# Performance work log

Measured on AMD Instinct MI355X. Metric: run time of the kernel, lower is better.

Reference implementation:

```python
import jax, jax.numpy as jnp
import numpy as np

B, S, W = 64, 128, 20
VOCAB, E, H = 256, 64, 256


def setup_inputs() -> dict:
    key = jax.random.key(0)
    ks = jax.random.split(key, 10)
    return {
        "chars": jax.random.randint(ks[0], (B, S, W), 0, VOCAB),
        "emb": jax.random.uniform(ks[1], (VOCAB, E), jnp.float32, -0.32, 0.32),
        "w1": jax.random.normal(ks[2], (H, E, 1), jnp.float32) * 0.1,
        "b1": jax.random.normal(ks[3], (H,), jnp.float32) * 0.1,
        "w3": jax.random.normal(ks[4], (H, E, 3), jnp.float32) * 0.1,
        "b3": jax.random.normal(ks[5], (H,), jnp.float32) * 0.1,
        "w5": jax.random.normal(ks[6], (H, E, 5), jnp.float32) * 0.1,
        "b5": jax.random.normal(ks[7], (H,), jnp.float32) * 0.1,
        "lw": jax.random.normal(ks[8], (H, 3 * H), jnp.float32) * 0.05,
        "lb": jax.random.normal(ks[9], (H,), jnp.float32) * 0.05,
    }


def _conv_relu_maxpool(x, w, b):
    # x: [N, E, W], w: [H, E, k] ('same' padding k//2) -> [N, H]
    k = w.shape[-1]
    pad = k // 2
    y = jax.lax.conv_general_dilated(
        x, w, window_strides=(1,), padding=[(pad, pad)],
        dimension_numbers=("NCH", "OIH", "NCH"))
    y = jax.nn.relu(y + b[None, :, None])
    return jnp.max(y, axis=2)  # global max over char positions


def reference(chars, emb, w1, b1, w3, b3, w5, b5, lw, lb):
    b, s, wlen = chars.shape
    flat = chars.reshape(-1, wlen)                 # [N, W]
    x = emb[flat]                                  # [N, W, E]
    x = jnp.transpose(x, (0, 2, 1))                # [N, E, W]
    outs = jnp.concatenate([
        _conv_relu_maxpool(x, w1, b1),
        _conv_relu_maxpool(x, w3, b3),
        _conv_relu_maxpool(x, w5, b5),
    ], axis=1)                                     # [N, 3H]
    out = outs @ lw.T + lb                         # [N, H]
    return out.reshape(b, s, -1)
```

## Files before the change

### kernel.cpp

```cpp
#include <hip/hip_runtime.h>
#include <hip/hip_bf16.h>

#define BB 64
#define SS 128
#define WW 20
#define NW (BB*SS)
#define VOCAB 256
#define EE 64
#define HH 256
#define K3 (3*HH)
#define NTAP 9
#define UNIT 2304

typedef short bf16x8 __attribute__((ext_vector_type(8)));
typedef float f32x4  __attribute__((ext_vector_type(4)));

__device__ __forceinline__ ushort f2bs(float x) {
    __hip_bfloat16 h = __float2bfloat16(x);
    union { __hip_bfloat16 h; ushort u; } c; c.h = h; return c.u;
}
__device__ __forceinline__ float blo(unsigned u) {
    union { unsigned i; float f; } c; c.i = u << 16; return c.f;
}
__device__ __forceinline__ float bhi(unsigned u) {
    union { unsigned i; float f; } c; c.i = u & 0xffff0000u; return c.f;
}

#define SET4(d, w0, w1) { d[0]=blo(w0); d[1]=bhi(w0); d[2]=blo(w1); d[3]=bhi(w1); }
#define ADD4(d, w0, w1) { d[0]+=blo(w0); d[1]+=bhi(w0); d[2]+=blo(w1); d[3]+=bhi(w1); }
#define MAX4(m, s) { m[0]=fmaxf(m[0],s[0]); m[1]=fmaxf(m[1],s[1]); \
                     m[2]=fmaxf(m[2],s[2]); m[3]=fmaxf(m[3],s[3]); }


__global__ __launch_bounds__(256) void prep(
        const float* __restrict__ w1,
        const float* __restrict__ w3,
        const float* __restrict__ w5,
        const float* __restrict__ lw,
        float* __restrict__ wTp,
        ushort* __restrict__ lwb) {
    const int bid = blockIdx.x;
    if (bid < 576) {
        int idx = bid * 256 + threadIdx.x;
        int e = idx / UNIT;
        int j = idx - e * UNIT;
        int tap, h;
        if (j < 2048) {
            int chunk = j >> 9, w = j & 511, p = w & 7;
            tap = chunk * 2 + (p >> 2);
            h   = (w >> 3) * 4 + (p & 3);
        } else { tap = 8; h = j - 2048; }
        float v;
        if (tap == 0)      v = w1[h*EE + e];
        else if (tap <= 3) v = w3[(h*EE + e)*3 + (tap-1)];
        else               v = w5[(h*EE + e)*5 + (tap-4)];
        wTp[idx] = v;
    } else {
        int i = ((bid - 576) * 256 + threadIdx.x) * 4;
        float4 v = *(const float4*)(lw + i);
        ushort4 o;
        o.x = f2bs(v.x); o.y = f2bs(v.y); o.z = f2bs(v.z); o.w = f2bs(v.w);
        *(ushort4*)(lwb + i) = o;
    }
}

__global__ __launch_bounds__(256) void build_tables(
        const float* __restrict__ emb,
        const float* __restrict__ wTp,
        ushort* __restrict__ P2) {
    __shared__ float emb_s[2][EE];
    const int v0 = blockIdx.x * 2;
    const int j  = blockIdx.y * 256 + threadIdx.x;
    const int t  = threadIdx.x;
    if (t < 2*EE) emb_s[t >> 6][t & 63] = emb[v0*EE + t];
    __syncthreads();

    float a0 = 0.f, a1 = 0.f;
    const float* wp = wTp + j;
    #pragma unroll 8
    for (int e = 0; e < EE; ++e) {
        float w = wp[e * UNIT];
        a0 += emb_s[0][e] * w;
        a1 += emb_s[1][e] * w;
    }
    P2[(size_t)(v0+0)*UNIT + j] = f2bs(a0);
    P2[(size_t)(v0+1)*UNIT + j] = f2bs(a1);
}

__global__ __launch_bounds__(256) void conv_pool(
        const int* __restrict__ chars,
        const ushort* __restrict__ P2,
        const float* __restrict__ b1,
        const float* __restrict__ b3,
        const float* __restrict__ b5,
        ushort* __restrict__ outs) {
    const int tid  = threadIdx.x;
    const int wave = tid >> 6, lane = tid & 63;
    const int n    = blockIdx.x * 4 + wave;
    const char* Pb = (const char*)P2;

    const int* cp = chars + n * WW;
    int c[WW];
    #pragma unroll
    for (int j = 0; j < WW; ++j) c[j] = __builtin_amdgcn_readfirstlane(cp[j]);

    float acc3[3][4], acc5[5][4], m1[4], m3[4], m5[4];
    #pragma unroll
    for (int i = 0; i < 4; ++i) {
        acc3[0][i] = 0.f; acc5[0][i] = 0.f; acc5[1][i] = 0.f;
        m1[i] = -1e30f; m3[i] = -1e30f; m5[i] = -1e30f;
    }

    uint4 q[2][4]; uint2 e8[2];
    {
        const char* p = Pb + (size_t)c[0] * 4608;
        #pragma unroll
        for (int i = 0; i < 4; ++i) q[0][i] = *(const uint4*)(p + i*1024 + lane*16);
        e8[0] = *(const uint2*)(p + 4096 + lane*8);
    }

    #pragma unroll
    for (int j = 0; j < WW; ++j) {
        const int cur = j & 1, nxt = cur ^ 1;
        if (j + 1 < WW) {
            const char* p = Pb + (size_t)c[j+1] * 4608;
            #pragma unroll
            for (int i = 0; i < 4; ++i) q[nxt][i] = *(const uint4*)(p + i*1024 + lane*16);
            e8[nxt] = *(const uint2*)(p + 4096 + lane*8);
        }
        uint4 q0 = q[cur][0], q1 = q[cur][1], q2 = q[cur][2], q3 = q[cur][3];
        uint2 ee = e8[cur];

        m1[0] = fmaxf(m1[0], blo(q0.x)); m1[1] = fmaxf(m1[1], bhi(q0.x));
        m1[2] = fmaxf(m1[2], blo(q0.y)); m1[3] = fmaxf(m1[3], bhi(q0.y));
        if (j + 1 < WW) SET4(acc3[(j+1)%3], q0.z, q0.w)
        ADD4(acc3[j%3], q1.x, q1.y)
        if (j >= 1) { ADD4(acc3[(j-1)%3], q1.z, q1.w)
                      MAX4(m3, acc3[(j-1)%3]) }
        if (j + 2 < WW) SET4(acc5[(j+2)%5], q2.x, q2.y)
        if (j + 1 < WW) ADD4(acc5[(j+1)%5], q2.z, q2.w)
        ADD4(acc5[j%5], q3.x, q3.y)
        if (j >= 1) ADD4(acc5[(j-1)%5], q3.z, q3.w)
        if (j >= 2) { ADD4(acc5[(j-2)%5], ee.x, ee.y)
                      MAX4(m5, acc5[(j-2)%5]) }
    }
    MAX4(m3, acc3[(WW-1)%3])
    MAX4(m5, acc5[(WW-2)%5])
    MAX4(m5, acc5[(WW-1)%5])

    const int h4 = lane * 4;
    float4 bb1 = *(const float4*)(b1 + h4);
    float4 bb3 = *(const float4*)(b3 + h4);
    float4 bb5 = *(const float4*)(b5 + h4);
    ushort* op = outs + (size_t)n * K3 + h4;
    ushort4 o;
    o.x = f2bs(fmaxf(m1[0]+bb1.x, 0.f)); o.y = f2bs(fmaxf(m1[1]+bb1.y, 0.f));
    o.z = f2bs(fmaxf(m1[2]+bb1.z, 0.f)); o.w = f2bs(fmaxf(m1[3]+bb1.w, 0.f));
    *(ushort4*)(op + 0*HH) = o;
    o.x = f2bs(fmaxf(m3[0]+bb3.x, 0.f)); o.y = f2bs(fmaxf(m3[1]+bb3.y, 0.f));
    o.z = f2bs(fmaxf(m3[2]+bb3.z, 0.f)); o.w = f2bs(fmaxf(m3[3]+bb3.w, 0.f));
    *(ushort4*)(op + 1*HH) = o;
    o.x = f2bs(fmaxf(m5[0]+bb5.x, 0.f)); o.y = f2bs(fmaxf(m5[1]+bb5.y, 0.f));
    o.z = f2bs(fmaxf(m5[2]+bb5.z, 0.f)); o.w = f2bs(fmaxf(m5[3]+bb5.w, 0.f));
    *(ushort4*)(op + 2*HH) = o;
}

__global__ __launch_bounds__(64) void gemm_out(
        const ushort* __restrict__ outs,
        const ushort* __restrict__ lwb,
        const float* __restrict__ lb,
        float* __restrict__ out) {
    const int lane = threadIdx.x;
    const int m0 = blockIdx.x * 32;
    const int n0 = blockIdx.y * 32;
    const int mrow = lane & 15, quad = lane >> 4;

    f32x4 acc00 = (f32x4){0,0,0,0}, acc01 = (f32x4){0,0,0,0};
    f32x4 acc10 = (f32x4){0,0,0,0}, acc11 = (f32x4){0,0,0,0};
    const ushort* ap = outs + (size_t)(m0 + mrow) * K3 + quad * 8;
    const ushort* bp = lwb  + (size_t)(n0 + mrow) * K3 + quad * 8;

    bf16x8 a0 = *(const bf16x8*)ap, a1 = *(const bf16x8*)(ap + 16*K3);
    bf16x8 b0 = *(const bf16x8*)bp, b1 = *(const bf16x8*)(bp + 16*K3);

    #pragma unroll
    for (int it = 0; it < K3/32; ++it) {
        const int kn = (it + 1 < K3/32) ? (it + 1) * 32 : 0;
        bf16x8 a0n = *(const bf16x8*)(ap + kn);
        bf16x8 a1n = *(const bf16x8*)(ap + 16*K3 + kn);
        bf16x8 b0n = *(const bf16x8*)(bp + kn);
        bf16x8 b1n = *(const bf16x8*)(bp + 16*K3 + kn);
        acc00 = __builtin_amdgcn_mfma_f32_16x16x32_bf16(a0, b0, acc00, 0, 0, 0);
        acc01 = __builtin_amdgcn_mfma_f32_16x16x32_bf16(a0, b1, acc01, 0, 0, 0);
        acc10 = __builtin_amdgcn_mfma_f32_16x16x32_bf16(a1, b0, acc10, 0, 0, 0);
        acc11 = __builtin_amdgcn_mfma_f32_16x16x32_bf16(a1, b1, acc11, 0, 0, 0);
        a0 = a0n; a1 = a1n; b0 = b0n; b1 = b1n;
    }

    #pragma unroll
    for (int i = 0; i < 2; ++i) {
        #pragma unroll
        for (int jn = 0; jn < 2; ++jn) {
            const f32x4 acc = (i==0) ? (jn==0 ? acc00 : acc01)
                                     : (jn==0 ? acc10 : acc11);
            int ncol = n0 + jn*16 + mrow;
            float lbv = lb[ncol];
            #pragma unroll
            for (int r = 0; r < 4; ++r)
                out[(size_t)(m0 + i*16 + quad*4 + r)*HH + ncol] = acc[r] + lbv;
        }
    }
}

extern "C" void kernel_launch(void* const* d_in, const int* in_sizes, int n_in,
                              void* d_out, int out_size, void* d_ws, size_t ws_size,
                              hipStream_t stream) {
    const int*   chars = (const int*)d_in[0];
    const float* emb   = (const float*)d_in[1];
    const float* w1    = (const float*)d_in[2];
    const float* b1    = (const float*)d_in[3];
    const float* w3    = (const float*)d_in[4];
    const float* b3    = (const float*)d_in[5];
    const float* w5    = (const float*)d_in[6];
    const float* b5    = (const float*)d_in[7];
    const float* lw    = (const float*)d_in[8];
    const float* lb    = (const float*)d_in[9];

    ushort* P2   = (ushort*)d_ws;
    float*  wTp  = (float*)(P2 + VOCAB * UNIT);
    ushort* outs = (ushort*)(wTp + EE * UNIT);
    ushort* lwb  = outs + (size_t)NW * K3;

    prep<<<768, 256, 0, stream>>>(w1, w3, w5, lw, wTp, lwb);
    build_tables<<<dim3(VOCAB/2, NTAP), 256, 0, stream>>>(emb, wTp, P2);
    conv_pool<<<NW/4, 256, 0, stream>>>(chars, P2, b1, b3, b5, outs);
    gemm_out<<<dim3(NW/32, HH/32), 64, 0, stream>>>(outs, lwb, lb, (float*)d_out);
}
```

Measured before the change: 141.5 us.

## Split conv_pool channels across two waves per word and shrink GEMM tiles

Reorders the precomputed per-character tap table into two 128-channel halves so each word is handled by two waves, each producing two channels per lane instead of four. Character indices are loaded with one vector load plus readlane, and the kernel gets an occupancy hint. build_tables now processes four vocab rows per block. The output GEMM uses 16-row tiles to launch more blocks. The aim is more parallelism and lower register pressure, at the cost of more waves reading the same character data and less reuse of B per GEMM block.

```diff
diff --git a/kernel.cpp b/kernel.cpp
--- a/kernel.cpp
+++ b/kernel.cpp
@@ -1,14 +1,12 @@
 #include <hip/hip_runtime.h>
 #include <hip/hip_bf16.h>
 
-#define BB 64
-#define SS 128
 #define WW 20
-#define NW (BB*SS)
+#define NW 8192
 #define VOCAB 256
 #define EE 64
 #define HH 256
-#define K3 (3*HH)
+#define K3 768
 #define NTAP 9
 #define UNIT 2304
 
@@ -25,11 +23,13 @@
 __device__ __forceinline__ float bhi(unsigned u) {
     union { unsigned i; float f; } c; c.i = u & 0xffff0000u; return c.f;
 }
-
-#define SET4(d, w0, w1) { d[0]=blo(w0); d[1]=bhi(w0); d[2]=blo(w1); d[3]=bhi(w1); }
-#define ADD4(d, w0, w1) { d[0]+=blo(w0); d[1]+=bhi(w0); d[2]+=blo(w1); d[3]+=bhi(w1); }
-#define MAX4(m, s) { m[0]=fmaxf(m[0],s[0]); m[1]=fmaxf(m[1],s[1]); \
-                     m[2]=fmaxf(m[2],s[2]); m[3]=fmaxf(m[3],s[3]); }
+__device__ __forceinline__ unsigned pack2(float lo, float hi) {
+    return (unsigned)f2bs(lo) | ((unsigned)f2bs(hi) << 16);
+}
+
+#define SET2(d, w) { d[0] = blo(w); d[1] = bhi(w); }
+#define ADD2(d, w) { d[0] += blo(w); d[1] += bhi(w); }
+#define MAX2(m, s) { m[0] = fmaxf(m[0], s[0]); m[1] = fmaxf(m[1], s[1]); }
 
 
 __global__ __launch_bounds__(256) void prep(
@@ -44,12 +44,14 @@
         int idx = bid * 256 + threadIdx.x;
         int e = idx / UNIT;
         int j = idx - e * UNIT;
+        int o  = j / 1152;
+        int jh = j - o * 1152;
         int tap, h;
-        if (j < 2048) {
-            int chunk = j >> 9, w = j & 511, p = w & 7;
-            tap = chunk * 2 + (p >> 2);
-            h   = (w >> 3) * 4 + (p & 3);
-        } else { tap = 8; h = j - 2048; }
+        if (jh < 1024) {
+            int c = jh >> 8, q = jh & 255, u = q >> 2, p = q & 3;
+            tap = 2*c + (p >> 1);
+            h   = o*128 + 2*u + (p & 1);
+        } else { tap = 8; h = o*128 + (jh - 1024); }
         float v;
         if (tap == 0)      v = w1[h*EE + e];
         else if (tap <= 3) v = w3[(h*EE + e)*3 + (tap-1)];
@@ -58,111 +60,106 @@
     } else {
         int i = ((bid - 576) * 256 + threadIdx.x) * 4;
         float4 v = *(const float4*)(lw + i);
-        ushort4 o;
-        o.x = f2bs(v.x); o.y = f2bs(v.y); o.z = f2bs(v.z); o.w = f2bs(v.w);
-        *(ushort4*)(lwb + i) = o;
+        ushort4 o4;
+        o4.x = f2bs(v.x); o4.y = f2bs(v.y); o4.z = f2bs(v.z); o4.w = f2bs(v.w);
+        *(ushort4*)(lwb + i) = o4;
     }
 }
 
 __global__ __launch_bounds__(256) void build_tables(
         const float* __restrict__ emb,
         const float* __restrict__ wTp,
-        ushort* __restrict__ P2) {
-    __shared__ float emb_s[2][EE];
-    const int v0 = blockIdx.x * 2;
+        ushort* __restrict__ P3) {
+    __shared__ float emb_s[4][EE];
+    const int v0 = blockIdx.x * 4;
     const int j  = blockIdx.y * 256 + threadIdx.x;
     const int t  = threadIdx.x;
-    if (t < 2*EE) emb_s[t >> 6][t & 63] = emb[v0*EE + t];
+    emb_s[t >> 6][t & 63] = emb[v0*EE + t];
     __syncthreads();
 
-    float a0 = 0.f, a1 = 0.f;
+    float a0 = 0.f, a1 = 0.f, a2 = 0.f, a3 = 0.f;
     const float* wp = wTp + j;
     #pragma unroll 8
     for (int e = 0; e < EE; ++e) {
         float w = wp[e * UNIT];
-        a0 += emb_s[0][e] * w;
-        a1 += emb_s[1][e] * w;
-    }
-    P2[(size_t)(v0+0)*UNIT + j] = f2bs(a0);
-    P2[(size_t)(v0+1)*UNIT + j] = f2bs(a1);
-}
-
-__global__ __launch_bounds__(256) void conv_pool(
+        a0 += emb_s[0][e] * w; a1 += emb_s[1][e] * w;
+        a2 += emb_s[2][e] * w; a3 += emb_s[3][e] * w;
+    }
+    P3[(size_t)(v0+0)*UNIT + j] = f2bs(a0);
+    P3[(size_t)(v0+1)*UNIT + j] = f2bs(a1);
+    P3[(size_t)(v0+2)*UNIT + j] = f2bs(a2);
+    P3[(size_t)(v0+3)*UNIT + j] = f2bs(a3);
+}
+
+__global__ __launch_bounds__(256, 8) void conv_pool(
         const int* __restrict__ chars,
-        const ushort* __restrict__ P2,
+        const ushort* __restrict__ P3,
         const float* __restrict__ b1,
         const float* __restrict__ b3,
         const float* __restrict__ b5,
         ushort* __restrict__ outs) {
     const int tid  = threadIdx.x;
     const int wave = tid >> 6, lane = tid & 63;
-    const int n    = blockIdx.x * 4 + wave;
-    const char* Pb = (const char*)P2;
-
-    const int* cp = chars + n * WW;
+    const int n    = blockIdx.x * 2 + (wave >> 1);
+    const int o    = wave & 1;
+
+    int cv = chars[n * WW + (lane < WW ? lane : WW - 1)];
     int c[WW];
     #pragma unroll
-    for (int j = 0; j < WW; ++j) c[j] = __builtin_amdgcn_readfirstlane(cp[j]);
-
-    float acc3[3][4], acc5[5][4], m1[4], m3[4], m5[4];
-    #pragma unroll
-    for (int i = 0; i < 4; ++i) {
-        acc3[0][i] = 0.f; acc5[0][i] = 0.f; acc5[1][i] = 0.f;
-        m1[i] = -1e30f; m3[i] = -1e30f; m5[i] = -1e30f;
-    }
-
-    uint4 q[2][4]; uint2 e8[2];
+    for (int j = 0; j < WW; ++j) c[j] = __builtin_amdgcn_readlane(cv, j);
+
+    const ushort* base = P3 + o * 1152;
+
+    float acc3[3][2], acc5[5][2], m1[2], m3[2], m5[2];
+    acc3[0][0]=0.f; acc3[0][1]=0.f;
+    acc5[0][0]=0.f; acc5[0][1]=0.f; acc5[1][0]=0.f; acc5[1][1]=0.f;
+    m1[0]=-1e30f; m1[1]=-1e30f; m3[0]=-1e30f; m3[1]=-1e30f;
+    m5[0]=-1e30f; m5[1]=-1e30f;
+
+    uint2 q[2][4]; unsigned t8[2];
     {
-        const char* p = Pb + (size_t)c[0] * 4608;
+        const ushort* p = base + (size_t)c[0] * UNIT;
         #pragma unroll
-        for (int i = 0; i < 4; ++i) q[0][i] = *(const uint4*)(p + i*1024 + lane*16);
-        e8[0] = *(const uint2*)(p + 4096 + lane*8);
+        for (int i = 0; i < 4; ++i) q[0][i] = *(const uint2*)(p + i*256 + lane*4);
+        t8[0] = *(const unsigned*)(p + 1024 + lane*2);
     }
 
     #pragma unroll
     for (int j = 0; j < WW; ++j) {
         const int cur = j & 1, nxt = cur ^ 1;
         if (j + 1 < WW) {
-            const char* p = Pb + (size_t)c[j+1] * 4608;
+            const ushort* p = base + (size_t)c[j+1] * UNIT;
             #pragma unroll
-            for (int i = 0; i < 4; ++i) q[nxt][i] = *(const uint4*)(p + i*1024 + lane*16);
-            e8[nxt] = *(const uint2*)(p + 4096 + lane*8);
+            for (int i = 0; i < 4; ++i) q[nxt][i] = *(const uint2*)(p + i*256 + lane*4);
+            t8[nxt] = *(const unsigned*)(p + 1024 + lane*2);
         }
-        uint4 q0 = q[cur][0], q1 = q[cur][1], q2 = q[cur][2], q3 = q[cur][3];
-        uint2 ee = e8[cur];
+        uint2 q0 = q[cur][0], q1 = q[cur][1], q2 = q[cur][2], q3 = q[cur][3];
+        unsigned e8 = t8[cur];
 
         m1[0] = fmaxf(m1[0], blo(q0.x)); m1[1] = fmaxf(m1[1], bhi(q0.x));
-        m1[2] = fmaxf(m1[2], blo(q0.y)); m1[3] = fmaxf(m1[3], bhi(q0.y));
-        if (j + 1 < WW) SET4(acc3[(j+1)%3], q0.z, q0.w)
-        ADD4(acc3[j%3], q1.x, q1.y)
-        if (j >= 1) { ADD4(acc3[(j-1)%3], q1.z, q1.w)
-                      MAX4(m3, acc3[(j-1)%3]) }
-        if (j + 2 < WW) SET4(acc5[(j+2)%5], q2.x, q2.y)
-        if (j + 1 < WW) ADD4(acc5[(j+1)%5], q2.z, q2.w)
-        ADD4(acc5[j%5], q3.x, q3.y)
-        if (j >= 1) ADD4(acc5[(j-1)%5], q3.z, q3.w)
-        if (j >= 2) { ADD4(acc5[(j-2)%5], ee.x, ee.y)
-                      MAX4(m5, acc5[(j-2)%5]) }
-    }
-    MAX4(m3, acc3[(WW-1)%3])
-    MAX4(m5, acc5[(WW-2)%5])
-    MAX4(m5, acc5[(WW-1)%5])
-
-    const int h4 = lane * 4;
-    float4 bb1 = *(const float4*)(b1 + h4);
-    float4 bb3 = *(const float4*)(b3 + h4);
-    float4 bb5 = *(const float4*)(b5 + h4);
-    ushort* op = outs + (size_t)n * K3 + h4;
-    ushort4 o;
-    o.x = f2bs(fmaxf(m1[0]+bb1.x, 0.f)); o.y = f2bs(fmaxf(m1[1]+bb1.y, 0.f));
-    o.z = f2bs(fmaxf(m1[2]+bb1.z, 0.f)); o.w = f2bs(fmaxf(m1[3]+bb1.w, 0.f));
-    *(ushort4*)(op + 0*HH) = o;
-    o.x = f2bs(fmaxf(m3[0]+bb3.x, 0.f)); o.y = f2bs(fmaxf(m3[1]+bb3.y, 0.f));
-    o.z = f2bs(fmaxf(m3[2]+bb3.z, 0.f)); o.w = f2bs(fmaxf(m3[3]+bb3.w, 0.f));
-    *(ushort4*)(op + 1*HH) = o;
-    o.x = f2bs(fmaxf(m5[0]+bb5.x, 0.f)); o.y = f2bs(fmaxf(m5[1]+bb5.y, 0.f));
-    o.z = f2bs(fmaxf(m5[2]+bb5.z, 0.f)); o.w = f2bs(fmaxf(m5[3]+bb5.w, 0.f));
-    *(ushort4*)(op + 2*HH) = o;
+        if (j + 1 < WW) SET2(acc3[(j+1)%3], q0.y)
+        ADD2(acc3[j%3], q1.x)
+        if (j >= 1) { ADD2(acc3[(j-1)%3], q1.y)
+                      MAX2(m3, acc3[(j-1)%3]) }
+        if (j + 2 < WW) SET2(acc5[(j+2)%5], q2.x)
+        if (j + 1 < WW) ADD2(acc5[(j+1)%5], q2.y)
+        ADD2(acc5[j%5], q3.x)
+        if (j >= 1) ADD2(acc5[(j-1)%5], q3.y)
+        if (j >= 2) { ADD2(acc5[(j-2)%5], e8)
+                      MAX2(m5, acc5[(j-2)%5]) }
+    }
+    MAX2(m3, acc3[(WW-1)%3])
+    MAX2(m5, acc5[(WW-2)%5])
+    MAX2(m5, acc5[(WW-1)%5])
+
+    const int h0 = o*128 + lane*2;
+    float2 bb1 = *(const float2*)(b1 + h0);
+    float2 bb3 = *(const float2*)(b3 + h0);
+    float2 bb5 = *(const float2*)(b5 + h0);
+    unsigned* op = (unsigned*)(outs + (size_t)n * K3 + h0);
+    op[0*(HH/2)] = pack2(fmaxf(m1[0]+bb1.x, 0.f), fmaxf(m1[1]+bb1.y, 0.f));
+    op[1*(HH/2)] = pack2(fmaxf(m3[0]+bb3.x, 0.f), fmaxf(m3[1]+bb3.y, 0.f));
+    op[2*(HH/2)] = pack2(fmaxf(m5[0]+bb5.x, 0.f), fmaxf(m5[1]+bb5.y, 0.f));
 }
 
 __global__ __launch_bounds__(64) void gemm_out(
@@ -171,44 +168,37 @@
         const float* __restrict__ lb,
         float* __restrict__ out) {
     const int lane = threadIdx.x;
-    const int m0 = blockIdx.x * 32;
+    const int m0 = blockIdx.x * 16;
     const int n0 = blockIdx.y * 32;
     const int mrow = lane & 15, quad = lane >> 4;
 
-    f32x4 acc00 = (f32x4){0,0,0,0}, acc01 = (f32x4){0,0,0,0};
-    f32x4 acc10 = (f32x4){0,0,0,0}, acc11 = (f32x4){0,0,0,0};
+    f32x4 acc0 = (f32x4){0,0,0,0}, acc1 = (f32x4){0,0,0,0};
     const ushort* ap = outs + (size_t)(m0 + mrow) * K3 + quad * 8;
     const ushort* bp = lwb  + (size_t)(n0 + mrow) * K3 + quad * 8;
 
-    bf16x8 a0 = *(const bf16x8*)ap, a1 = *(const bf16x8*)(ap + 16*K3);
-    bf16x8 b0 = *(const bf16x8*)bp, b1 = *(const bf16x8*)(bp + 16*K3);
+    bf16x8 a  = *(const bf16x8*)ap;
+    bf16x8 b0 = *(const bf16x8*)bp;
+    bf16x8 b1 = *(const bf16x8*)(bp + 16*K3);
 
     #pragma unroll
     for (int it = 0; it < K3/32; ++it) {
         const int kn = (it + 1 < K3/32) ? (it + 1) * 32 : 0;
-        bf16x8 a0n = *(const bf16x8*)(ap + kn);
-        bf16x8 a1n = *(const bf16x8*)(ap + 16*K3 + kn);
+        bf16x8 an  = *(const bf16x8*)(ap + kn);
         bf16x8 b0n = *(const bf16x8*)(bp + kn);
         bf16x8 b1n = *(const bf16x8*)(bp + 16*K3 + kn);
-        acc00 = __builtin_amdgcn_mfma_f32_16x16x32_bf16(a0, b0, acc00, 0, 0, 0);
-        acc01 = __builtin_amdgcn_mfma_f32_16x16x32_bf16(a0, b1, acc01, 0, 0, 0);
-        acc10 = __builtin_amdgcn_mfma_f32_16x16x32_bf16(a1, b0, acc10, 0, 0, 0);
-        acc11 = __builtin_amdgcn_mfma_f32_16x16x32_bf16(a1, b1, acc11, 0, 0, 0);
-        a0 = a0n; a1 = a1n; b0 = b0n; b1 = b1n;
-    }
-
-    #pragma unroll
-    for (int i = 0; i < 2; ++i) {
+        acc0 = __builtin_amdgcn_mfma_f32_16x16x32_bf16(a, b0, acc0, 0, 0, 0);
+        acc1 = __builtin_amdgcn_mfma_f32_16x16x32_bf16(a, b1, acc1, 0, 0, 0);
+        a = an; b0 = b0n; b1 = b1n;
+    }
+
+    #pragma unroll
+    for (int nn = 0; nn < 2; ++nn) {
+        const f32x4 acc = nn ? acc1 : acc0;
+        int ncol = n0 + nn*16 + mrow;
+        float lbv = lb[ncol];
         #pragma unroll
-        for (int jn = 0; jn < 2; ++jn) {
-            const f32x4 acc = (i==0) ? (jn==0 ? acc00 : acc01)
-                                     : (jn==0 ? acc10 : acc11);
-            int ncol = n0 + jn*16 + mrow;
-            float lbv = lb[ncol];
-            #pragma unroll
-            for (int r = 0; r < 4; ++r)
-                out[(size_t)(m0 + i*16 + quad*4 + r)*HH + ncol] = acc[r] + lbv;
-        }
+        for (int r = 0; r < 4; ++r)
+            out[(size_t)(m0 + quad*4 + r)*HH + ncol] = acc[r] + lbv;
     }
 }
 
@@ -226,13 +216,13 @@
     const float* lw    = (const float*)d_in[8];
     const float* lb    = (const float*)d_in[9];
 
-    ushort* P2   = (ushort*)d_ws;
-    float*  wTp  = (float*)(P2 + VOCAB * UNIT);
+    ushort* P3   = (ushort*)d_ws;
+    float*  wTp  = (float*)(P3 + VOCAB * UNIT);
     ushort* outs = (ushort*)(wTp + EE * UNIT);
     ushort* lwb  = outs + (size_t)NW * K3;
 
     prep<<<768, 256, 0, stream>>>(w1, w3, w5, lw, wTp, lwb);
-    build_tables<<<dim3(VOCAB/2, NTAP), 256, 0, stream>>>(emb, wTp, P2);
-    conv_pool<<<NW/4, 256, 0, stream>>>(chars, P2, b1, b3, b5, outs);
-    gemm_out<<<dim3(NW/32, HH/32), 64, 0, stream>>>(outs, lwb, lb, (float*)d_out);
-}
+    build_tables<<<dim3(VOCAB/4, NTAP), 256, 0, stream>>>(emb, wTp, P3);
+    conv_pool<<<NW/2, 256, 0, stream>>>(chars, P3, b1, b3, b5, outs);
+    gemm_out<<<dim3(NW/16, HH/32), 64, 0, stream>>>(outs, lwb, lb, (float*)d_out);
+}
```

Result: slower. 262.6 us (+85.6%).
